# Optimization experiments

Measured on AMD Instinct MI355X. Metric: run time of the kernel, lower is better.

## Reference

```python
import jax, jax.numpy as jnp
import numpy as np
from jax import lax

GEN_POLY = ("1111001", "1011011")  # rate 1/2, constraint length 7 (octal 171/133)


def build_trellis(gen_poly):
    """Feed-forward (non-recursive) convolutional trellis tables.

    State = shift-register contents, most-recent bit is the MSB of the state
    index. Returns int32 tables, each [ns, ni]:
      to_nodes[s, b]        : next state from state s with input bit b
      op_by_fromnode[s, b]  : emitted output-symbol index for (s, b)
      from_nodes[j, m]      : m-th predecessor state of state j
      ip_by_tonode[j, m]    : input bit taken on that predecessor transition
    """
    mu = len(gen_poly[0]) - 1
    ns, ni = 2 ** mu, 2
    g = np.array([[int(c) for c in p] for p in gen_poly])  # [conv_n, mu+1]
    to_nodes = np.zeros((ns, ni), np.int32)
    op_by_fromnode = np.zeros((ns, ni), np.int32)
    from_nodes = np.zeros((ns, ni), np.int32)
    ip_by_tonode = np.zeros((ns, ni), np.int32)
    fill = np.zeros(ns, np.int32)
    for s in range(ns):
        rbits = [(s >> (mu - 1 - j)) & 1 for j in range(mu)]
        for b in range(ni):
            w = np.array([b] + rbits)                 # full window [b, r0..r_{mu-1}]
            obits = (g @ w) % 2                        # output bits, MSB first
            o = int("".join(str(int(x)) for x in obits), 2)
            j = int("".join(str(x) for x in ([b] + rbits[:-1])), 2)
            to_nodes[s, b] = j
            op_by_fromnode[s, b] = o
            from_nodes[j, fill[j]] = s
            ip_by_tonode[j, fill[j]] = b
            fill[j] += 1
    return to_nodes, op_by_fromnode, from_nodes, ip_by_tonode


TO_NODES, OP_BY_FROM, FROM_NODES, IP_BY_TO = build_trellis(GEN_POLY)
CONV_N = len(GEN_POLY)
MU = len(GEN_POLY[0]) - 1
NS = 2 ** MU
NO = 2 ** CONV_N
# output-symbol bit patterns, MSB first, mapped to signs (1-2*bit)
_OP_BITS = np.array([[(o >> (CONV_N - 1 - j)) & 1 for j in range(CONV_N)]
                     for o in range(NO)], np.float32)
OP_SIGN = jnp.asarray(1.0 - 2.0 * _OP_BITS)  # [NO, CONV_N]
IP_SIGN = jnp.asarray([1.0, -1.0])           # sign of input bit b: 1-2b


def setup_inputs() -> dict:
    key = jax.random.key(0)
    k1, k2 = jax.random.split(key)
    B, n = 256, 4096
    T = n // CONV_N  # = k = 2048 info bits
    llr_ch = jax.random.normal(k1, (B, n), dtype=jnp.float32)
    llr_a = jax.random.normal(k2, (B, T), dtype=jnp.float32)
    return {"llr_ch": llr_ch, "llr_a": llr_a}


def _bcjr(llr_ch, llr_a):
    B, n = llr_ch.shape
    T = n // CONV_N
    # branch metrics: bm[t, b, o] = exp(0.5 * sum_j llr[b, t, j] * (1-2*opbit_j(o)))
    llr_r = llr_ch.reshape(B, T, CONV_N)
    bm = jnp.exp(0.5 * jnp.einsum('btj,oj->tbo', llr_r, OP_SIGN))  # [T, B, NO]
    llr_a_t = llr_a.T  # [T, B]

    def gamma_fn(bm_t, la_t):
        # a-priori factor exp(0.5*llr_a*(1-2b)) times channel branch metric
        ap = jnp.exp(0.5 * la_t[:, None, None] * IP_SIGN[None, None, :])  # [B,1,2]
        return ap * bm_t[:, OP_BY_FROM]  # [B, NS, 2]

    alpha0 = jnp.zeros((B, NS), jnp.float32).at[:, 0].set(1.0)

    def fwd(alpha_prev, inp):
        bm_t, la_t = inp
        gam = gamma_fn(bm_t, la_t)                        # [B, NS, 2] by from-state
        ag = gam * alpha_prev[:, :, None]                  # alpha_{t} * gamma_t
        agt = ag[:, FROM_NODES, IP_BY_TO]                  # regroup by to-state
        alpha = agt.sum(-1)
        alpha = alpha / alpha.sum(-1, keepdims=True)       # normalize (as in TF code)
        return alpha, alpha_prev                            # emit alpha BEFORE step t

    _, alphas = lax.scan(fwd, alpha0, (bm, llr_a_t))       # alphas[t] = alpha_t, [T,B,NS]

    beta_T = jnp.full((B, NS), 1.0 / NS, jnp.float32)      # non-terminated: uniform

    def bwd(beta_next, inp):
        bm_t, la_t, alpha_t = inp
        gam = gamma_fn(bm_t, la_t)                         # [B, NS, 2]
        bg = gam * beta_next[:, TO_NODES]                  # gamma * beta_{t+1}(to)
        beta = bg.sum(-1)
        beta = beta / beta.sum(-1, keepdims=True)
        joint = alpha_t[:, :, None] * bg                   # APP per (state, bit)
        llr_t = jnp.log(joint[..., 0].sum(-1)) - jnp.log(joint[..., 1].sum(-1))
        return beta, llr_t

    _, llrs_rev = lax.scan(bwd, beta_T, (bm[::-1], llr_a_t[::-1], alphas[::-1]))
    return llrs_rev[::-1].T  # [B, T] soft LLRs (hard_out=False)


def reference(llr_ch, llr_a):
    return _bcjr(llr_ch, llr_a)
```

## Files before the change

kernel.cpp:

```cpp
#include <hip/hip_runtime.h>
#include <hip/hip_bf16.h>

#define T_LEN 2048
#define NSTATE 64
#define NCHUNK 16
#define CH_S 128
#define WARM 64
#define RK 16

__device__ __forceinline__ float wave_sum64(float v) {
    #pragma unroll
    for (int d = 1; d < 64; d <<= 1) v += __shfl_xor(v, d, 64);
    return v;
}

__device__ __forceinline__ float pair_sum_xor1(float v) {
    int r = __builtin_amdgcn_update_dpp(0, __float_as_int(v), 0xB1, 0xF, 0xF, true);
    return v + __int_as_float(r);
}

__device__ __forceinline__ unsigned short bf16_of(float f) {
    return (unsigned short)((__float_as_uint(f) + 0x8000u) >> 16);
}
__device__ __forceinline__ float bf16_lo(unsigned u) { return __uint_as_float(u << 16); }
__device__ __forceinline__ float bf16_hi(unsigned u) { return __uint_as_float(u & 0xffff0000u); }


__global__ __launch_bounds__(256, 8)
void bcjr_sweep_kernel(const float* __restrict__ llr_ch,
                       const float* __restrict__ llr_a,
                       unsigned short* __restrict__ wsA,
                       unsigned short* __restrict__ wsB)
{
    const int wave  = blockIdx.x * 4 + (threadIdx.x >> 6);
    const int lane  = threadIdx.x & 63;
    const int dir   = wave & 1;
    const int chunk = (wave >> 1) & (NCHUNK - 1);
    const int b     = wave >> 5;

    const float c0 = 1.0f - 2.0f * (float)(__popc(lane & 57) & 1);
    const float c1 = 1.0f - 2.0f * (float)(__popc(lane & 27) & 1);
    const float kE = 0.5f * 1.442695040888963f;
    const float k0 = kE * c0, k1 = kE * c1;

    const float* chp = llr_ch + (size_t)b * (2 * T_LEN);
    const float* lap = llr_a  + (size_t)b * T_LEN;

    if (dir == 0) {
        unsigned short* w = wsA + (size_t)b * T_LEN * NSTATE;
        const int  fs0 = 2 * (lane & 31);
        const bool fhi = (lane >= 32);
        const int t0 = chunk * CH_S;
        const int ts = (chunk == 0) ? t0 : t0 - WARM;
        float state = (chunk == 0) ? ((lane == 0) ? 1.0f : 0.0f) : (1.0f / 64.0f);

        for (int g = ts; g < t0 + CH_S; g += RK) {
            const bool store = (g >= t0);
            #pragma unroll
            for (int h = 0; h < 2; ++h) {
                const int gb = g + 8 * h;
                const float4* c4 = (const float4*)(chp + 2 * gb);
                const float4* a4 = (const float4*)(lap + gb);
                float4 cc[4], aa[2];
                #pragma unroll
                for (int i = 0; i < 4; ++i) cc[i] = c4[i];
                #pragma unroll
                for (int i = 0; i < 2; ++i) aa[i] = a4[i];
                unsigned short* wb = w + (size_t)gb * NSTATE + lane;
                #pragma unroll
                for (int i = 0; i < 8; ++i) {
                    float l0 = (i & 1) ? cc[i >> 1].z : cc[i >> 1].x;
                    float l1 = (i & 1) ? cc[i >> 1].w : cc[i >> 1].y;
                    float la = ((const float*)aa)[i];
                    if (store) wb[i * NSTATE] = bf16_of(state);
                    float x   = fmaf(la, kE, fmaf(l0, k0, l1 * k1));
                    float g0v = exp2f(x);
                    float g1v = __builtin_amdgcn_rcpf(g0v);
                    float s0  = pair_sum_xor1(state * g0v);
                    float s1  = pair_sum_xor1(state * g1v);
                    float a0  = __shfl(s0, fs0, 64);
                    float a1  = __shfl(s1, fs0, 64);
                    state = fhi ? a1 : a0;
                }
            }
            float s = wave_sum64(state);
            state = state * __builtin_amdgcn_rcpf(s);
        }
    } else {
        unsigned short* w = wsB + (size_t)b * T_LEN * NSTATE;
        const int bs0 = lane >> 1;
        const int bs1 = 32 + (lane >> 1);
        const int t0 = chunk * CH_S;
        const int te = (chunk == NCHUNK - 1) ? (t0 + CH_S) : (t0 + CH_S + WARM);
        float state = 1.0f / 64.0f;

        for (int g = te - RK; g >= t0; g -= RK) {
            const bool store = (g < t0 + CH_S);
            #pragma unroll
            for (int h = 1; h >= 0; --h) {
                const int gb = g + 8 * h;
                const float4* c4 = (const float4*)(chp + 2 * gb);
                const float4* a4 = (const float4*)(lap + gb);
                float4 cc[4], aa[2];
                #pragma unroll
                for (int i = 0; i < 4; ++i) cc[i] = c4[i];
                #pragma unroll
                for (int i = 0; i < 2; ++i) aa[i] = a4[i];
                unsigned short* wb = w + (size_t)gb * NSTATE + lane;
                #pragma unroll
                for (int i = 7; i >= 0; --i) {
                    float l0 = (i & 1) ? cc[i >> 1].z : cc[i >> 1].x;
                    float l1 = (i & 1) ? cc[i >> 1].w : cc[i >> 1].y;
                    float la = ((const float*)aa)[i];
                    if (store) wb[i * NSTATE] = bf16_of(state);
                    float x   = fmaf(la, kE, fmaf(l0, k0, l1 * k1));
                    float g0v = exp2f(x);
                    float g1v = __builtin_amdgcn_rcpf(g0v);
                    float t0v = __shfl(state, bs0, 64);
                    float t1v = __shfl(state, bs1, 64);
                    state = fmaf(g0v, t0v, g1v * t1v);
                }
            }
            float s = wave_sum64(state);
            state = state * __builtin_amdgcn_rcpf(s);
        }
    }
}

__global__ __launch_bounds__(256, 4)
void bcjr_llr_kernel(const float* __restrict__ llr_ch,
                     const float* __restrict__ llr_a,
                     const unsigned short* __restrict__ wsA,
                     const unsigned short* __restrict__ wsB,
                     float* __restrict__ out)
{
    const int gid = blockIdx.x * 256 + threadIdx.x;

    const uint4* ap = (const uint4*)(wsA + (size_t)gid * NSTATE);
    const uint4* bp = (const uint4*)(wsB + (size_t)gid * NSTATE);

    unsigned Bw[32];
    #pragma unroll
    for (int k = 0; k < 8; ++k) {
        uint4 v = bp[k];
        Bw[4 * k] = v.x; Bw[4 * k + 1] = v.y; Bw[4 * k + 2] = v.z; Bw[4 * k + 3] = v.w;
    }

    float2 c2 = ((const float2*)llr_ch)[gid];
    float  la = llr_a[gid];
    const float kE = 0.5f * 1.442695040888963f;
    float E = la * kE, X0 = c2.x * kE, X1 = c2.y * kE;

    float G[4], R[4];
    G[0] = exp2f(E + X0 + X1);
    G[1] = exp2f(E + X0 - X1);
    G[2] = exp2f(E - X0 + X1);
    G[3] = exp2f(E - X0 - X1);
    #pragma unroll
    for (int k = 0; k < 4; ++k) R[k] = __builtin_amdgcn_rcpf(G[k]);

    float n0 = 0.0f, n1 = 0.0f;
    #pragma unroll
    for (int k = 0; k < 8; ++k) {
        uint4 av = ap[k];
        unsigned aw[4] = { av.x, av.y, av.z, av.w };
        #pragma unroll
        for (int m = 0; m < 4; ++m) {
            const int j = 4 * k + m;
            const int k0 = ((__popc(j & 28) & 1) << 1) | (__popc(j & 13) & 1);
            float a0 = bf16_lo(aw[m]);
            float a1 = bf16_hi(aw[m]);
            unsigned bd0 = Bw[j >> 1];
            unsigned bd1 = Bw[16 + (j >> 1)];
            float b0 = (j & 1) ? bf16_hi(bd0) : bf16_lo(bd0);
            float b1 = (j & 1) ? bf16_hi(bd1) : bf16_lo(bd1);
            n0 = fmaf(b0, fmaf(a0, G[k0], a1 * G[k0 ^ 3]), n0);
            n1 = fmaf(b1, fmaf(a0, R[k0], a1 * R[k0 ^ 3]), n1);
        }
    }
    out[gid] = __logf(n0) - __logf(n1);
}

extern "C" void kernel_launch(void* const* d_in, const int* in_sizes, int n_in,
                              void* d_out, int out_size, void* d_ws, size_t ws_size,
                              hipStream_t stream) {
    const float* llr_ch = (const float*)d_in[0];
    const float* llr_a  = (const float*)d_in[1];
    float* out = (float*)d_out;

    int B = in_sizes[0] / (2 * T_LEN);
    const size_t traj_bytes = (size_t)B * T_LEN * NSTATE * sizeof(unsigned short);

    unsigned short* wsA = (unsigned short*)d_ws;
    unsigned short* wsB = (unsigned short*)((char*)d_ws + traj_bytes);

    int n_waves = B * NCHUNK * 2;
    hipLaunchKernelGGL(bcjr_sweep_kernel, dim3(n_waves / 4), dim3(256), 0, stream,
                       llr_ch, llr_a, wsA, wsB);

    int n_thr = B * T_LEN;
    hipLaunchKernelGGL(bcjr_llr_kernel, dim3(n_thr / 256), dim3(256), 0, stream,
                       llr_ch, llr_a, wsA, wsB, out);
}
```

Measured before the change: 147.1 us.

## Fuse forward/backward sweeps and LLR computation into one kernel via LDS

Replaces the two-kernel design, which wrote bf16 alpha and beta trajectories to global workspace and then read them back in a separate LLR kernel, with one fused kernel per (batch, chunk) block of two waves. Wave 0 runs the forward recursion and stores alpha in LDS. Meanwhile wave 1 runs only the backward warm-up. After a barrier, wave 1 runs the real backward pass and computes each LLR inline using two wave-wide reductions per step. This removes the global trajectory round trip and the second launch. In exchange, the backward pass is now serialized after the forward pass, and it adds two 64-lane shuffle reductions plus two logs per time step on the critical path.

```diff
diff --git a/kernel.cpp b/kernel.cpp
--- a/kernel.cpp
+++ b/kernel.cpp
@@ -1,8 +1,6 @@
 #include <hip/hip_runtime.h>
-#include <hip/hip_bf16.h>
 
 #define T_LEN 2048
-#define NSTATE 64
 #define NCHUNK 16
 #define CH_S 128
 #define WARM 64
@@ -22,21 +20,19 @@
 __device__ __forceinline__ unsigned short bf16_of(float f) {
     return (unsigned short)((__float_as_uint(f) + 0x8000u) >> 16);
 }
-__device__ __forceinline__ float bf16_lo(unsigned u) { return __uint_as_float(u << 16); }
-__device__ __forceinline__ float bf16_hi(unsigned u) { return __uint_as_float(u & 0xffff0000u); }
 
+__global__ __launch_bounds__(128, 4)
+void bcjr_fused(const float* __restrict__ llr_ch,
+                const float* __restrict__ llr_a,
+                float* __restrict__ out)
+{
+    __shared__ unsigned short lds_a[CH_S * 64];
 
-__global__ __launch_bounds__(256, 8)
-void bcjr_sweep_kernel(const float* __restrict__ llr_ch,
-                       const float* __restrict__ llr_a,
-                       unsigned short* __restrict__ wsA,
-                       unsigned short* __restrict__ wsB)
-{
-    const int wave  = blockIdx.x * 4 + (threadIdx.x >> 6);
+    const int blk   = blockIdx.x;
+    const int b     = blk >> 4;
+    const int chunk = blk & (NCHUNK - 1);
+    const int wave  = threadIdx.x >> 6;
     const int lane  = threadIdx.x & 63;
-    const int dir   = wave & 1;
-    const int chunk = (wave >> 1) & (NCHUNK - 1);
-    const int b     = wave >> 5;
 
     const float c0 = 1.0f - 2.0f * (float)(__popc(lane & 57) & 1);
     const float c1 = 1.0f - 2.0f * (float)(__popc(lane & 27) & 1);
@@ -45,14 +41,18 @@
 
     const float* chp = llr_ch + (size_t)b * (2 * T_LEN);
     const float* lap = llr_a  + (size_t)b * T_LEN;
+    const int t0 = chunk * CH_S;
 
-    if (dir == 0) {
-        unsigned short* w = wsA + (size_t)b * T_LEN * NSTATE;
+    const int bs0 = lane >> 1;
+    const int bs1 = 32 + (lane >> 1);
+
+    float state;
+
+    if (wave == 0) {
         const int  fs0 = 2 * (lane & 31);
         const bool fhi = (lane >= 32);
-        const int t0 = chunk * CH_S;
         const int ts = (chunk == 0) ? t0 : t0 - WARM;
-        float state = (chunk == 0) ? ((lane == 0) ? 1.0f : 0.0f) : (1.0f / 64.0f);
+        state = (chunk == 0) ? ((lane == 0) ? 1.0f : 0.0f) : (1.0f / 64.0f);
 
         for (int g = ts; g < t0 + CH_S; g += RK) {
             const bool store = (g >= t0);
@@ -61,18 +61,17 @@
                 const int gb = g + 8 * h;
                 const float4* c4 = (const float4*)(chp + 2 * gb);
                 const float4* a4 = (const float4*)(lap + gb);
-                float4 cc[4], aa[2];
+                float4 cc[4]; float4 aa[2];
                 #pragma unroll
                 for (int i = 0; i < 4; ++i) cc[i] = c4[i];
                 #pragma unroll
                 for (int i = 0; i < 2; ++i) aa[i] = a4[i];
-                unsigned short* wb = w + (size_t)gb * NSTATE + lane;
                 #pragma unroll
                 for (int i = 0; i < 8; ++i) {
                     float l0 = (i & 1) ? cc[i >> 1].z : cc[i >> 1].x;
                     float l1 = (i & 1) ? cc[i >> 1].w : cc[i >> 1].y;
                     float la = ((const float*)aa)[i];
-                    if (store) wb[i * NSTATE] = bf16_of(state);
+                    if (store) lds_a[(gb - t0 + i) * 64 + lane] = bf16_of(state);
                     float x   = fmaf(la, kE, fmaf(l0, k0, l1 * k1));
                     float g0v = exp2f(x);
                     float g1v = __builtin_amdgcn_rcpf(g0v);
@@ -87,98 +86,80 @@
             state = state * __builtin_amdgcn_rcpf(s);
         }
     } else {
-        unsigned short* w = wsB + (size_t)b * T_LEN * NSTATE;
-        const int bs0 = lane >> 1;
-        const int bs1 = 32 + (lane >> 1);
-        const int t0 = chunk * CH_S;
-        const int te = (chunk == NCHUNK - 1) ? (t0 + CH_S) : (t0 + CH_S + WARM);
-        float state = 1.0f / 64.0f;
+        state = 1.0f / 64.0f;
+        if (chunk != NCHUNK - 1) {
+            for (int g = t0 + CH_S + WARM - RK; g >= t0 + CH_S; g -= RK) {
+                #pragma unroll
+                for (int h = 1; h >= 0; --h) {
+                    const int gb = g + 8 * h;
+                    const float4* c4 = (const float4*)(chp + 2 * gb);
+                    const float4* a4 = (const float4*)(lap + gb);
+                    float4 cc[4]; float4 aa[2];
+                    #pragma unroll
+                    for (int i = 0; i < 4; ++i) cc[i] = c4[i];
+                    #pragma unroll
+                    for (int i = 0; i < 2; ++i) aa[i] = a4[i];
+                    #pragma unroll
+                    for (int i = 7; i >= 0; --i) {
+                        float l0 = (i & 1) ? cc[i >> 1].z : cc[i >> 1].x;
+                        float l1 = (i & 1) ? cc[i >> 1].w : cc[i >> 1].y;
+                        float la = ((const float*)aa)[i];
+                        float x   = fmaf(la, kE, fmaf(l0, k0, l1 * k1));
+                        float g0v = exp2f(x);
+                        float g1v = __builtin_amdgcn_rcpf(g0v);
+                        float t0v = __shfl(state, bs0, 64);
+                        float t1v = __shfl(state, bs1, 64);
+                        state = fmaf(g0v, t0v, g1v * t1v);
+                    }
+                }
+                float s = wave_sum64(state);
+                state = state * __builtin_amdgcn_rcpf(s);
+            }
+        }
+    }
 
-        for (int g = te - RK; g >= t0; g -= RK) {
-            const bool store = (g < t0 + CH_S);
+    __syncthreads();
+
+    if (wave == 1) {
+        float* outp = out + (size_t)b * T_LEN;
+        float keep = 0.0f;
+        for (int g = t0 + CH_S - RK; g >= t0; g -= RK) {
             #pragma unroll
             for (int h = 1; h >= 0; --h) {
                 const int gb = g + 8 * h;
                 const float4* c4 = (const float4*)(chp + 2 * gb);
                 const float4* a4 = (const float4*)(lap + gb);
-                float4 cc[4], aa[2];
+                float4 cc[4]; float4 aa[2];
                 #pragma unroll
                 for (int i = 0; i < 4; ++i) cc[i] = c4[i];
                 #pragma unroll
                 for (int i = 0; i < 2; ++i) aa[i] = a4[i];
-                unsigned short* wb = w + (size_t)gb * NSTATE + lane;
                 #pragma unroll
                 for (int i = 7; i >= 0; --i) {
+                    const int t = gb + i;
                     float l0 = (i & 1) ? cc[i >> 1].z : cc[i >> 1].x;
                     float l1 = (i & 1) ? cc[i >> 1].w : cc[i >> 1].y;
                     float la = ((const float*)aa)[i];
-                    if (store) wb[i * NSTATE] = bf16_of(state);
                     float x   = fmaf(la, kE, fmaf(l0, k0, l1 * k1));
                     float g0v = exp2f(x);
                     float g1v = __builtin_amdgcn_rcpf(g0v);
                     float t0v = __shfl(state, bs0, 64);
                     float t1v = __shfl(state, bs1, 64);
-                    state = fmaf(g0v, t0v, g1v * t1v);
+                    float bg0 = g0v * t0v;
+                    float bg1 = g1v * t1v;
+                    float ar = __uint_as_float(((unsigned)lds_a[(t - t0) * 64 + lane]) << 16);
+                    float n0 = wave_sum64(ar * bg0);
+                    float n1 = wave_sum64(ar * bg1);
+                    float llr = __logf(n0) - __logf(n1);
+                    keep = (lane == (t & 63)) ? llr : keep;
+                    state = bg0 + bg1;
                 }
             }
+            if ((g & 63) == 0) outp[g + lane] = keep;
             float s = wave_sum64(state);
             state = state * __builtin_amdgcn_rcpf(s);
         }
     }
-}
-
-__global__ __launch_bounds__(256, 4)
-void bcjr_llr_kernel(const float* __restrict__ llr_ch,
-                     const float* __restrict__ llr_a,
-                     const unsigned short* __restrict__ wsA,
-                     const unsigned short* __restrict__ wsB,
-                     float* __restrict__ out)
-{
-    const int gid = blockIdx.x * 256 + threadIdx.x;
-
-    const uint4* ap = (const uint4*)(wsA + (size_t)gid * NSTATE);
-    const uint4* bp = (const uint4*)(wsB + (size_t)gid * NSTATE);
-
-    unsigned Bw[32];
-    #pragma unroll
-    for (int k = 0; k < 8; ++k) {
-        uint4 v = bp[k];
-        Bw[4 * k] = v.x; Bw[4 * k + 1] = v.y; Bw[4 * k + 2] = v.z; Bw[4 * k + 3] = v.w;
-    }
-
-    float2 c2 = ((const float2*)llr_ch)[gid];
-    float  la = llr_a[gid];
-    const float kE = 0.5f * 1.442695040888963f;
-    float E = la * kE, X0 = c2.x * kE, X1 = c2.y * kE;
-
-    float G[4], R[4];
-    G[0] = exp2f(E + X0 + X1);
-    G[1] = exp2f(E + X0 - X1);
-    G[2] = exp2f(E - X0 + X1);
-    G[3] = exp2f(E - X0 - X1);
-    #pragma unroll
-    for (int k = 0; k < 4; ++k) R[k] = __builtin_amdgcn_rcpf(G[k]);
-
-    float n0 = 0.0f, n1 = 0.0f;
-    #pragma unroll
-    for (int k = 0; k < 8; ++k) {
-        uint4 av = ap[k];
-        unsigned aw[4] = { av.x, av.y, av.z, av.w };
-        #pragma unroll
-        for (int m = 0; m < 4; ++m) {
-            const int j = 4 * k + m;
-            const int k0 = ((__popc(j & 28) & 1) << 1) | (__popc(j & 13) & 1);
-            float a0 = bf16_lo(aw[m]);
-            float a1 = bf16_hi(aw[m]);
-            unsigned bd0 = Bw[j >> 1];
-            unsigned bd1 = Bw[16 + (j >> 1)];
-            float b0 = (j & 1) ? bf16_hi(bd0) : bf16_lo(bd0);
-            float b1 = (j & 1) ? bf16_hi(bd1) : bf16_lo(bd1);
-            n0 = fmaf(b0, fmaf(a0, G[k0], a1 * G[k0 ^ 3]), n0);
-            n1 = fmaf(b1, fmaf(a0, R[k0], a1 * R[k0 ^ 3]), n1);
-        }
-    }
-    out[gid] = __logf(n0) - __logf(n1);
 }
 
 extern "C" void kernel_launch(void* const* d_in, const int* in_sizes, int n_in,
@@ -189,16 +170,6 @@
     float* out = (float*)d_out;
 
     int B = in_sizes[0] / (2 * T_LEN);
-    const size_t traj_bytes = (size_t)B * T_LEN * NSTATE * sizeof(unsigned short);
-
-    unsigned short* wsA = (unsigned short*)d_ws;
-    unsigned short* wsB = (unsigned short*)((char*)d_ws + traj_bytes);
-
-    int n_waves = B * NCHUNK * 2;
-    hipLaunchKernelGGL(bcjr_sweep_kernel, dim3(n_waves / 4), dim3(256), 0, stream,
-                       llr_ch, llr_a, wsA, wsB);
-
-    int n_thr = B * T_LEN;
-    hipLaunchKernelGGL(bcjr_llr_kernel, dim3(n_thr / 256), dim3(256), 0, stream,
-                       llr_ch, llr_a, wsA, wsB, out);
+    hipLaunchKernelGGL(bcjr_fused, dim3(B * NCHUNK), dim3(128), 0, stream,
+                       llr_ch, llr_a, out);
 }
```

New measurement: 214.3 us. 45.7% more time.

## Split LLR combine across 8 lanes per time step with shuffle reduction

Applied to the files above, without the earlier changes.

The LLR kernel now gives each time step to 8 threads instead of one. Each thread loads a contiguous 16-byte slice of alpha and two 8-byte slices of beta, so the wave's loads coalesce instead of striding through 128-byte rows per thread. The 8 partial sums are combined with xor shuffles. The gamma terms are computed per lane from parity-flipped signs and an exp(2E) identity, which replaces four exponentials per step. This costs 8x more threads, redundant loads of the channel inputs, and a small shuffle reduction.

```diff
diff --git a/kernel.cpp b/kernel.cpp
--- a/kernel.cpp
+++ b/kernel.cpp
@@ -127,7 +127,7 @@
     }
 }
 
-__global__ __launch_bounds__(256, 4)
+__global__ __launch_bounds__(256, 8)
 void bcjr_llr_kernel(const float* __restrict__ llr_ch,
                      const float* __restrict__ llr_a,
                      const unsigned short* __restrict__ wsA,
@@ -135,50 +135,59 @@
                      float* __restrict__ out)
 {
     const int gid = blockIdx.x * 256 + threadIdx.x;
-
-    const uint4* ap = (const uint4*)(wsA + (size_t)gid * NSTATE);
-    const uint4* bp = (const uint4*)(wsB + (size_t)gid * NSTATE);
-
-    unsigned Bw[32];
-    #pragma unroll
-    for (int k = 0; k < 8; ++k) {
-        uint4 v = bp[k];
-        Bw[4 * k] = v.x; Bw[4 * k + 1] = v.y; Bw[4 * k + 2] = v.z; Bw[4 * k + 3] = v.w;
-    }
-
-    float2 c2 = ((const float2*)llr_ch)[gid];
-    float  la = llr_a[gid];
+    const int rt  = gid >> 3;
+    const int q   = gid & 7;
+
+    const uint4 av = ((const uint4*)(wsA + (size_t)rt * NSTATE))[q];
+    const uint2 b0 = ((const uint2*)(wsB + (size_t)rt * NSTATE))[q];
+    const uint2 b1 = ((const uint2*)(wsB + (size_t)rt * NSTATE + 32))[q];
+
+    float2 c2 = ((const float2*)llr_ch)[rt];
+    float  la = llr_a[rt];
     const float kE = 0.5f * 1.442695040888963f;
     float E = la * kE, X0 = c2.x * kE, X1 = c2.y * kE;
 
-    float G[4], R[4];
-    G[0] = exp2f(E + X0 + X1);
-    G[1] = exp2f(E + X0 - X1);
-    G[2] = exp2f(E - X0 + X1);
-    G[3] = exp2f(E - X0 - X1);
-    #pragma unroll
-    for (int k = 0; k < 4; ++k) R[k] = __builtin_amdgcn_rcpf(G[k]);
+    const unsigned p0 = (unsigned)(__popc(q) & 1) << 31;
+    const unsigned p1 = (unsigned)(__popc(q & 3) & 1) << 31;
+    float sX0 = __uint_as_float(__float_as_uint(X0) ^ p0);
+    float sX1 = __uint_as_float(__float_as_uint(X1) ^ p1);
+
+    float Ge = exp2f(E + sX0 + sX1);
+    float Go = exp2f(E + sX0 - sX1);
+    float Re = __builtin_amdgcn_rcpf(Ge);
+    float Ro = __builtin_amdgcn_rcpf(Go);
+    float e2E = exp2f(E + E);
+    float r2E = __builtin_amdgcn_rcpf(e2E);
+    float GBe = e2E * Re, GBo = e2E * Ro;
+    float RBe = r2E * Ge, RBo = r2E * Go;
+
+    const unsigned aw[4]  = { av.x, av.y, av.z, av.w };
+    const unsigned bw0[2] = { b0.x, b0.y };
+    const unsigned bw1[2] = { b1.x, b1.y };
 
     float n0 = 0.0f, n1 = 0.0f;
     #pragma unroll
-    for (int k = 0; k < 8; ++k) {
-        uint4 av = ap[k];
-        unsigned aw[4] = { av.x, av.y, av.z, av.w };
-        #pragma unroll
-        for (int m = 0; m < 4; ++m) {
-            const int j = 4 * k + m;
-            const int k0 = ((__popc(j & 28) & 1) << 1) | (__popc(j & 13) & 1);
-            float a0 = bf16_lo(aw[m]);
-            float a1 = bf16_hi(aw[m]);
-            unsigned bd0 = Bw[j >> 1];
-            unsigned bd1 = Bw[16 + (j >> 1)];
-            float b0 = (j & 1) ? bf16_hi(bd0) : bf16_lo(bd0);
-            float b1 = (j & 1) ? bf16_hi(bd1) : bf16_lo(bd1);
-            n0 = fmaf(b0, fmaf(a0, G[k0], a1 * G[k0 ^ 3]), n0);
-            n1 = fmaf(b1, fmaf(a0, R[k0], a1 * R[k0 ^ 3]), n1);
-        }
+    for (int m = 0; m < 4; ++m) {
+        float GA = (m & 1) ? Go  : Ge;
+        float GB = (m & 1) ? GBo : GBe;
+        float RA = (m & 1) ? Ro  : Re;
+        float RB = (m & 1) ? RBo : RBe;
+        float a0 = bf16_lo(aw[m]);
+        float a1 = bf16_hi(aw[m]);
+        unsigned bd0 = bw0[m >> 1];
+        unsigned bd1 = bw1[m >> 1];
+        float b0v = (m & 1) ? bf16_hi(bd0) : bf16_lo(bd0);
+        float b1v = (m & 1) ? bf16_hi(bd1) : bf16_lo(bd1);
+        n0 = fmaf(b0v, fmaf(a0, GA, a1 * GB), n0);
+        n1 = fmaf(b1v, fmaf(a0, RA, a1 * RB), n1);
     }
-    out[gid] = __logf(n0) - __logf(n1);
+
+    #pragma unroll
+    for (int d = 1; d < 8; d <<= 1) {
+        n0 += __shfl_xor(n0, d, 64);
+        n1 += __shfl_xor(n1, d, 64);
+    }
+    if (q == 0) out[rt] = __logf(n0) - __logf(n1);
 }
 
 extern "C" void kernel_launch(void* const* d_in, const int* in_sizes, int n_in,
@@ -198,7 +207,7 @@
     hipLaunchKernelGGL(bcjr_sweep_kernel, dim3(n_waves / 4), dim3(256), 0, stream,
                        llr_ch, llr_a, wsA, wsB);
 
-    int n_thr = B * T_LEN;
+    int n_thr = B * T_LEN * 8;
     hipLaunchKernelGGL(bcjr_llr_kernel, dim3(n_thr / 256), dim3(256), 0, stream,
                        llr_ch, llr_a, wsA, wsB, out);
 }
```

Measured after the change: 131.6 us. -10.5%, faster.
